# Kernel optimization log

Hardware: AMD Instinct MI355X
Metric: run time of the kernel (lower is better)

The kernel has to match this reference:

```python
import jax, jax.numpy as jnp
import numpy as np

B, T, H, W = 8, 16, 512, 512
N, C = 300000, 128
STRIDE_B, STRIDE_T, STRIDE_H = T * H * W, H * W, W
SENTINEL = B * STRIDE_B  # out-of-range linear index used as unique fill_value


def setup_inputs() -> dict:
    key = jax.random.key(0)
    ks = jax.random.split(key, 8)
    # Random valid voxel coordinates via decomposed random linear index
    lin = jax.random.randint(ks[0], (N,), 0, SENTINEL, dtype=jnp.int32)
    b = lin // STRIDE_B
    r = lin % STRIDE_B
    t = r // STRIDE_T
    r = r % STRIDE_T
    y = r // STRIDE_H
    x = r % STRIDE_H
    indices = jnp.stack([b, t, y, x], axis=1).astype(jnp.int32)  # [N,4]
    s = 0.02
    return {
        "feats": jax.random.normal(ks[1], (N, C), jnp.float32),
        "indices": indices,
        "W1": jax.random.normal(ks[2], (C, C), jnp.float32) * s,
        "ln1_g": jnp.ones((C,), jnp.float32),
        "ln1_b": jnp.zeros((C,), jnp.float32),
        "W2": jax.random.normal(ks[3], (C, C), jnp.float32) * s,
        "ln2_g": jnp.ones((C,), jnp.float32),
        "ln2_b": jnp.zeros((C,), jnp.float32),
        "se_w1": jax.random.normal(ks[4], (C, C // 4), jnp.float32) * s,
        "se_b1": jnp.zeros((C // 4,), jnp.float32),
        "se_w2": jax.random.normal(ks[5], (C // 4, C), jnp.float32) * s,
        "se_b2": jnp.zeros((C,), jnp.float32),
    }


def _layernorm(x, g, b, eps=1e-5):
    mu = jnp.mean(x, axis=-1, keepdims=True)
    var = jnp.mean((x - mu) ** 2, axis=-1, keepdims=True)
    return (x - mu) * jax.lax.rsqrt(var + eps) * g + b


def reference(feats, indices, W1, ln1_g, ln1_b, W2, ln2_g, ln2_b,
              se_w1, se_b1, se_w2, se_b2):
    # conv1 (SubMConv3d k=1 == per-voxel linear) -> LayerNorm -> ReLU
    out = jax.nn.relu(_layernorm(feats @ W1, ln1_g, ln1_b))
    # conv2 -> LayerNorm
    out = _layernorm(out @ W2, ln2_g, ln2_b)
    # SE: global mean over all voxels -> fc -> relu -> fc -> sigmoid -> scale
    squeezed = jnp.mean(out, axis=0)                       # [C]
    scale = jax.nn.sigmoid(jax.nn.relu(squeezed @ se_w1 + se_b1) @ se_w2 + se_b2)
    out = out * scale
    # sparse_add(out, identity): linear hash, unique, scatter_add
    idx = indices.astype(jnp.int32)
    lin = (idx[:, 0] * STRIDE_B + idx[:, 1] * STRIDE_T
           + idx[:, 2] * STRIDE_H + idx[:, 3])             # [N]
    all_lin = jnp.concatenate([lin, lin])                  # [2N]
    all_feats = jnp.concatenate([out, feats])              # [2N, C]
    M = all_lin.shape[0]
    uniq, inv = jnp.unique(all_lin, size=M, fill_value=SENTINEL,
                           return_inverse=True)
    inv = inv.ravel()
    merged = jax.ops.segment_sum(all_feats, inv, num_segments=M)  # [2N, C]
    # decompose unique linear indices back to (b, t, y, x)
    cb = uniq // STRIDE_B
    r = uniq % STRIDE_B
    ct = r // STRIDE_T
    r = r % STRIDE_T
    ch = r // STRIDE_H
    cw = r % STRIDE_H
    comb_idx = jnp.stack([cb, ct, ch, cw], axis=1).astype(jnp.int32)
    # drop zero-feature / padded voxels (fixed-shape mask instead of compaction)
    valid = (jnp.abs(merged).sum(axis=1) > 1e-8) & (uniq < SENTINEL)
    merged = jnp.where(valid[:, None], merged, 0.0)
    merged = jax.nn.relu(merged)                           # lif2
    return merged, comb_idx, valid
```

## Files before the change

kernel.cpp:

```cpp
#include <hip/hip_runtime.h>
#include <cstdint>
#include <cstddef>

#define NVOX 300000
#define SB 4194304
#define ST 262144
#define SHH 512
#define SENT 33554432
#define NWORDS (SENT/64)

typedef __attribute__((ext_vector_type(8))) short short8;
typedef __attribute__((ext_vector_type(4))) float f32x4;

static __device__ __forceinline__ float bf2f(unsigned short u){
  return __uint_as_float(((unsigned)u) << 16);
}
static __device__ __forceinline__ unsigned short f2bf(float f){
  unsigned u = __float_as_uint(f);
  u = u + 0x7fffu + ((u >> 16) & 1u);
  return (unsigned short)(u >> 16);
}
static __device__ __forceinline__ short8 pack8(float4 a, float4 b){
  short8 s;
  s[0]=(short)f2bf(a.x); s[1]=(short)f2bf(a.y); s[2]=(short)f2bf(a.z); s[3]=(short)f2bf(a.w);
  s[4]=(short)f2bf(b.x); s[5]=(short)f2bf(b.y); s[6]=(short)f2bf(b.z); s[7]=(short)f2bf(b.w);
  return s;
}

static __device__ __forceinline__ unsigned rank_of(int l,
    const unsigned long long* __restrict__ bits,
    const unsigned* __restrict__ coarse,
    const unsigned* __restrict__ blockExcl){
  int w = l >> 6;
  unsigned long long m = 1ull << (l & 63);
  return coarse[w] + blockExcl[w >> 12]
       + (unsigned)__popcll(bits[w] & (m - 1ull));
}

__global__ void pack_w(const float* __restrict__ W, unsigned short* __restrict__ Wt){
  int i = blockIdx.x*256 + threadIdx.x;
  int j = i & 7, lane = (i >> 3) & 63, ks = (i >> 9) & 3, nt = i >> 11;
  int k = ks*32 + (lane >> 4)*8 + j;
  int n = nt*16 + (lane & 15);
  Wt[i] = f2bf(W[k*128 + n]);
}

__global__ void mark_kernel(const int* __restrict__ idx,
                            unsigned long long* __restrict__ bits,
                            unsigned long long* __restrict__ dupbits,
                            int* __restrict__ lin,
                            int* __restrict__ duplist,
                            int* __restrict__ dupcount){
  int i = blockIdx.x*256 + threadIdx.x;
  if(i >= NVOX) return;
  int4 v = ((const int4*)idx)[i];
  int l = v.x*SB + v.y*ST + v.z*SHH + v.w;
  lin[i] = l;
  unsigned long long m = 1ull << (l & 63);
  unsigned long long old = atomicOr(&bits[l >> 6], m);
  if(old & m){
    atomicOr(&dupbits[l >> 6], m);
    int s = atomicAdd(dupcount, 1);
    duplist[s] = i;
  }
}

__global__ void scan1_kernel(const unsigned long long* __restrict__ bits,
                             unsigned* __restrict__ coarse,
                             unsigned* __restrict__ blockSums){
  __shared__ unsigned sh[256];
  int t = threadIdx.x, blk = blockIdx.x;
  int w0 = blk*4096 + t*16;
  unsigned p[16]; unsigned s = 0;
  #pragma unroll
  for(int k=0;k<16;k++){ unsigned c = (unsigned)__popcll(bits[w0+k]); p[k] = s; s += c; }
  sh[t] = s; __syncthreads();
  for(int off=1; off<256; off<<=1){
    unsigned v = (t >= off) ? sh[t-off] : 0u;
    __syncthreads();
    sh[t] += v;
    __syncthreads();
  }
  unsigned texcl = (t == 0) ? 0u : sh[t-1];
  #pragma unroll
  for(int k=0;k<16;k++) coarse[w0+k] = texcl + p[k];
  if(t == 255) blockSums[blk] = sh[255];
}

__global__ void scan2_kernel(const unsigned* __restrict__ blockSums,
                             unsigned* __restrict__ blockExcl){
  __shared__ unsigned sh[128];
  int t = threadIdx.x;
  sh[t] = blockSums[t]; __syncthreads();
  for(int off=1; off<128; off<<=1){
    unsigned v = (t >= off) ? sh[t-off] : 0u;
    __syncthreads();
    sh[t] += v;
    __syncthreads();
  }
  if(t == 0) blockExcl[0] = 0u;
  blockExcl[t+1] = sh[t];
}

__global__ void emit_kernel(const unsigned long long* __restrict__ bits,
                            const unsigned* __restrict__ coarse,
                            const unsigned* __restrict__ blockExcl,
                            float* __restrict__ out_comb){
  int w = blockIdx.x*256 + threadIdx.x;
  if(w >= NWORDS) return;
  unsigned long long bw = bits[w];
  if(!bw) return;
  unsigned j = coarse[w] + blockExcl[w >> 12];
  while(bw){
    int p = __builtin_ctzll(bw);
    bw &= bw - 1;
    int v = (w << 6) | p;
    int cb = v >> 22;
    int r  = v & (SB - 1);
    int ct = r >> 18;
    r &= (ST - 1);
    int ch = r >> 9;
    int cw = r & 511;
    ((float4*)out_comb)[j] = make_float4((float)cb,(float)ct,(float)ch,(float)cw);
    j++;
  }
}

__global__ void zerodup_kernel(const int* __restrict__ duplist,
    const int* __restrict__ dupcount, const int* __restrict__ lin,
    const unsigned long long* __restrict__ bits,
    const unsigned* __restrict__ coarse, const unsigned* __restrict__ blockExcl,
    float* __restrict__ out_merged)
{
  int cnt = *dupcount;
  int lane = threadIdx.x & 63;
  for(int e = blockIdx.x*4 + (threadIdx.x >> 6); e < cnt; e += gridDim.x*4){
    int l = lin[duplist[e]];
    unsigned j = rank_of(l, bits, coarse, blockExcl);
    *(float2*)(out_merged + (size_t)j*128 + 2*lane) = make_float2(0.f, 0.f);
  }
}

#define MLP_ROWS 128
__global__ __launch_bounds__(256) void fused_mlp(
    const float* __restrict__ X,
    const unsigned short* __restrict__ w1t, const float* __restrict__ g1v,
    const float* __restrict__ b1v,
    const unsigned short* __restrict__ w2t, const float* __restrict__ g2v,
    const float* __restrict__ b2v,
    unsigned short* __restrict__ Y, float* __restrict__ sq, int nrows)
{
  __shared__ __align__(16) unsigned short wlds[16384];
  __shared__ __align__(16) unsigned short xs[128][136];
  __shared__ float sqs[4][128];
  const int t = threadIdx.x;
  const int rowbase = blockIdx.x * MLP_ROWS;
  const int wave = t >> 6, quad = (t >> 4) & 3, l15 = t & 15;
  const int wbase = wave * 32;
  const int lane8 = (t & 63) * 8;
  const int kofs = quad * 8;
  const int grow0 = rowbase + wbase + l15;
  const int grow1 = grow0 + 16;
  const bool rv0 = grow0 < nrows, rv1 = grow1 < nrows;

  #pragma unroll
  for (int m = 0; m < 8; m++)
    ((float4*)wlds)[m*256 + t] = ((const float4*)w1t)[m*256 + t];

  short8 a0,a1,a2,a3,a4,a5,a6,a7;
  {
    float4 z = make_float4(0.f,0.f,0.f,0.f);
    float4 u0=z,u1=z,u2=z,u3=z,u4=z,u5=z,u6=z,u7=z;
    float4 w0=z,w1=z,w2=z,w3=z,w4=z,w5=z,w6=z,w7=z;
    if (rv0) {
      const float* xp = X + (size_t)grow0 * 128 + kofs;
      u0 = ((const float4*)(xp      ))[0];
      u1 = ((const float4*)(xp +   4))[0];
      u2 = ((const float4*)(xp +  32))[0];
      u3 = ((const float4*)(xp +  36))[0];
      u4 = ((const float4*)(xp +  64))[0];
      u5 = ((const float4*)(xp +  68))[0];
      u6 = ((const float4*)(xp +  96))[0];
      u7 = ((const float4*)(xp + 100))[0];
    }
    if (rv1) {
      const float* xp = X + (size_t)grow1 * 128 + kofs;
      w0 = ((const float4*)(xp      ))[0];
      w1 = ((const float4*)(xp +   4))[0];
      w2 = ((const float4*)(xp +  32))[0];
      w3 = ((const float4*)(xp +  36))[0];
      w4 = ((const float4*)(xp +  64))[0];
      w5 = ((const float4*)(xp +  68))[0];
      w6 = ((const float4*)(xp +  96))[0];
      w7 = ((const float4*)(xp + 100))[0];
    }
    a0 = pack8(u0, u1); a1 = pack8(u2, u3);
    a2 = pack8(u4, u5); a3 = pack8(u6, u7);
    a4 = pack8(w0, w1); a5 = pack8(w2, w3);
    a6 = pack8(w4, w5); a7 = pack8(w6, w7);
  }
  __syncthreads();

  {
    f32x4 acc0[8], acc1[8];
    #pragma unroll
    for (int nt = 0; nt < 8; nt++) {
      const unsigned short* wp = wlds + nt*2048 + lane8;
      short8 bv0 = *(const short8*)(wp);
      short8 bv1 = *(const short8*)(wp + 512);
      short8 bv2 = *(const short8*)(wp + 1024);
      short8 bv3 = *(const short8*)(wp + 1536);
      f32x4 c0 = {0.f,0.f,0.f,0.f}, c1 = {0.f,0.f,0.f,0.f};
      c0 = __builtin_amdgcn_mfma_f32_16x16x32_bf16(a0, bv0, c0, 0, 0, 0);
      c1 = __builtin_amdgcn_mfma_f32_16x16x32_bf16(a4, bv0, c1, 0, 0, 0);
      c0 = __builtin_amdgcn_mfma_f32_16x16x32_bf16(a1, bv1, c0, 0, 0, 0);
      c1 = __builtin_amdgcn_mfma_f32_16x16x32_bf16(a5, bv1, c1, 0, 0, 0);
      c0 = __builtin_amdgcn_mfma_f32_16x16x32_bf16(a2, bv2, c0, 0, 0, 0);
      c1 = __builtin_amdgcn_mfma_f32_16x16x32_bf16(a6, bv2, c1, 0, 0, 0);
      c0 = __builtin_amdgcn_mfma_f32_16x16x32_bf16(a3, bv3, c0, 0, 0, 0);
      c1 = __builtin_amdgcn_mfma_f32_16x16x32_bf16(a7, bv3, c1, 0, 0, 0);
      acc0[nt] = c0; acc1[nt] = c1;
    }

    float gg[8], bb[8];
    #pragma unroll
    for (int nt = 0; nt < 8; nt++) {
      gg[nt] = g1v[nt*16 + l15]; bb[nt] = b1v[nt*16 + l15];
    }
    #pragma unroll
    for (int tile = 0; tile < 2; tile++) {
      #pragma unroll
      for (int r = 0; r < 4; r++) {
        float s = 0.f, q = 0.f;
        #pragma unroll
        for (int nt = 0; nt < 8; nt++) {
          float v = tile ? acc1[nt][r] : acc0[nt][r]; s += v; q += v*v;
        }
        #pragma unroll
        for (int mm = 1; mm < 16; mm <<= 1) { s += __shfl_xor(s, mm); q += __shfl_xor(q, mm); }
        float mu = s * (1.f/128.f);
        float var = fmaxf(q * (1.f/128.f) - mu*mu, 0.f);
        float rinv = rsqrtf(var + 1e-5f);
        int orow = wbase + tile*16 + quad*4 + r;
        #pragma unroll
        for (int nt = 0; nt < 8; nt++) {
          float v = ((tile ? acc1[nt][r] : acc0[nt][r]) - mu) * rinv * gg[nt] + bb[nt];
          v = fmaxf(v, 0.f);
          xs[orow][nt*16 + l15] = f2bf(v);
        }
      }
    }
  }
  __syncthreads();

  #pragma unroll
  for (int m = 0; m < 8; m++)
    ((float4*)wlds)[m*256 + t] = ((const float4*)w2t)[m*256 + t];

  short8 p0 = *(const short8*)&xs[wbase + l15][  0 + kofs];
  short8 p1 = *(const short8*)&xs[wbase + l15][ 32 + kofs];
  short8 p2 = *(const short8*)&xs[wbase + l15][ 64 + kofs];
  short8 p3 = *(const short8*)&xs[wbase + l15][ 96 + kofs];
  short8 p4 = *(const short8*)&xs[wbase + 16 + l15][  0 + kofs];
  short8 p5 = *(const short8*)&xs[wbase + 16 + l15][ 32 + kofs];
  short8 p6 = *(const short8*)&xs[wbase + 16 + l15][ 64 + kofs];
  short8 p7 = *(const short8*)&xs[wbase + 16 + l15][ 96 + kofs];
  __syncthreads();

  {
    f32x4 acc0[8], acc1[8];
    #pragma unroll
    for (int nt = 0; nt < 8; nt++) {
      const unsigned short* wp = wlds + nt*2048 + lane8;
      short8 bv0 = *(const short8*)(wp);
      short8 bv1 = *(const short8*)(wp + 512);
      short8 bv2 = *(const short8*)(wp + 1024);
      short8 bv3 = *(const short8*)(wp + 1536);
      f32x4 c0 = {0.f,0.f,0.f,0.f}, c1 = {0.f,0.f,0.f,0.f};
      c0 = __builtin_amdgcn_mfma_f32_16x16x32_bf16(p0, bv0, c0, 0, 0, 0);
      c1 = __builtin_amdgcn_mfma_f32_16x16x32_bf16(p4, bv0, c1, 0, 0, 0);
      c0 = __builtin_amdgcn_mfma_f32_16x16x32_bf16(p1, bv1, c0, 0, 0, 0);
      c1 = __builtin_amdgcn_mfma_f32_16x16x32_bf16(p5, bv1, c1, 0, 0, 0);
      c0 = __builtin_amdgcn_mfma_f32_16x16x32_bf16(p2, bv2, c0, 0, 0, 0);
      c1 = __builtin_amdgcn_mfma_f32_16x16x32_bf16(p6, bv2, c1, 0, 0, 0);
      c0 = __builtin_amdgcn_mfma_f32_16x16x32_bf16(p3, bv3, c0, 0, 0, 0);
      c1 = __builtin_amdgcn_mfma_f32_16x16x32_bf16(p7, bv3, c1, 0, 0, 0);
      acc0[nt] = c0; acc1[nt] = c1;
    }

    float gg[8], bb[8], ch[8];
    #pragma unroll
    for (int nt = 0; nt < 8; nt++) {
      gg[nt] = g2v[nt*16 + l15]; bb[nt] = b2v[nt*16 + l15]; ch[nt] = 0.f;
    }
    #pragma unroll
    for (int tile = 0; tile < 2; tile++) {
      #pragma unroll
      for (int r = 0; r < 4; r++) {
        float s = 0.f, q = 0.f;
        #pragma unroll
        for (int nt = 0; nt < 8; nt++) {
          float v = tile ? acc1[nt][r] : acc0[nt][r]; s += v; q += v*v;
        }
        #pragma unroll
        for (int mm = 1; mm < 16; mm <<= 1) { s += __shfl_xor(s, mm); q += __shfl_xor(q, mm); }
        float mu = s * (1.f/128.f);
        float var = fmaxf(q * (1.f/128.f) - mu*mu, 0.f);
        float rinv = rsqrtf(var + 1e-5f);
        int orow = wbase + tile*16 + quad*4 + r;
        bool rv = (rowbase + orow) < nrows;
        #pragma unroll
        for (int nt = 0; nt < 8; nt++) {
          float v = ((tile ? acc1[nt][r] : acc0[nt][r]) - mu) * rinv * gg[nt] + bb[nt];
          if (rv) ch[nt] += v;
          xs[orow][nt*16 + l15] = f2bf(v);
        }
      }
    }
    #pragma unroll
    for (int nt = 0; nt < 8; nt++) {
      float v = ch[nt];
      v += __shfl_xor(v, 16); v += __shfl_xor(v, 32);
      if (quad == 0) sqs[wave][nt*16 + l15] = v;
    }
  }

  #pragma unroll
  for (int mm = 0; mm < 8; mm++) {
    int c = mm*64 + (t & 63);
    int rl = wbase + (c >> 4), s8 = c & 15;
    if (rowbase + rl < nrows) {
      short8 v = *(const short8*)&xs[rl][s8*8];
      *(short8*)(Y + (size_t)(rowbase+rl)*128 + s8*8) = v;
    }
  }
  __syncthreads();
  if (t < 128) atomicAdd(&sq[t], sqs[0][t] + sqs[1][t] + sqs[2][t] + sqs[3][t]);
}

__global__ void se_kernel(const float* __restrict__ sq, const float* __restrict__ w1,
    const float* __restrict__ b1, const float* __restrict__ w2,
    const float* __restrict__ b2, float* __restrict__ scale)
{
  __shared__ float mean[128];
  __shared__ float h1[32];
  int t = threadIdx.x;
  mean[t] = sq[t] * (1.f/(float)NVOX);
  __syncthreads();
  if(t < 32){
    float s = b1[t];
    for(int c=0;c<128;c++) s += mean[c]*w1[c*32+t];
    h1[t] = fmaxf(s, 0.f);
  }
  __syncthreads();
  float s = b2[t];
  for(int j=0;j<32;j++) s += h1[j]*w2[j*128+t];
  scale[t] = 1.f/(1.f + expf(-s));
}

__global__ void scatter_kernel(const unsigned short* __restrict__ y2,
    const float* __restrict__ feats, const float* __restrict__ scale,
    const int* __restrict__ lin, const unsigned long long* __restrict__ bits,
    const unsigned long long* __restrict__ dupbits,
    const unsigned* __restrict__ coarse, const unsigned* __restrict__ blockExcl,
    float* __restrict__ out_merged, float* __restrict__ out_valid)
{
  int row = blockIdx.x*4 + (threadIdx.x >> 6);
  int lane = threadIdx.x & 63;
  int l = lin[row];
  int w = l >> 6;
  unsigned long long m = 1ull << (l & 63);
  unsigned j = coarse[w] + blockExcl[w >> 12]
             + (unsigned)__popcll(bits[w] & (m - 1ull));
  size_t rb = (size_t)row * 128;
  unsigned yy = *(const unsigned*)(y2 + rb + 2*lane);
  float2 ff = *(const float2*)(feats + rb + 2*lane);
  float2 ss = *(const float2*)(scale + 2*lane);
  float v0 = bf2f((unsigned short)(yy & 0xffffu)) * ss.x + ff.x;
  float v1 = bf2f((unsigned short)(yy >> 16))     * ss.y + ff.y;
  size_t ob = (size_t)j * 128;
  if (dupbits[w] & m) {
    atomicAdd(out_merged + ob + 2*lane,     v0);
    atomicAdd(out_merged + ob + 2*lane + 1, v1);
  } else {
    float s = fabsf(v0) + fabsf(v1);
    #pragma unroll
    for(int mm=1; mm<64; mm<<=1) s += __shfl_xor(s, mm);
    bool valid = s > 1e-8f;
    float2 o;
    o.x = valid ? fmaxf(v0, 0.f) : 0.f;
    o.y = valid ? fmaxf(v1, 0.f) : 0.f;
    *(float2*)(out_merged + ob + 2*lane) = o;
    if (lane == 0) out_valid[j] = valid ? 1.f : 0.f;
  }
}

__global__ void dupfinal_kernel(const int* __restrict__ duplist,
    const int* __restrict__ dupcount, const int* __restrict__ lin,
    unsigned long long* __restrict__ dupbits,
    const unsigned long long* __restrict__ bits,
    const unsigned* __restrict__ coarse, const unsigned* __restrict__ blockExcl,
    float* __restrict__ out_merged, float* __restrict__ out_valid)
{
  int cnt = *dupcount;
  int lane = threadIdx.x & 63;
  for(int e = blockIdx.x*4 + (threadIdx.x >> 6); e < cnt; e += gridDim.x*4){
    int l = lin[duplist[e]];
    int w = l >> 6;
    unsigned long long m = 1ull << (l & 63);
    int claimed = 0;
    if (lane == 0){
      unsigned long long old = atomicAnd(&dupbits[w], ~m);
      claimed = (old & m) ? 1 : 0;
    }
    claimed = __shfl(claimed, 0);
    if (!claimed) continue;
    unsigned j = coarse[w] + blockExcl[w >> 12]
               + (unsigned)__popcll(bits[w] & (m - 1ull));
    size_t ob = (size_t)j * 128;
    float2 v = *(float2*)(out_merged + ob + 2*lane);
    float s = fabsf(v.x) + fabsf(v.y);
    #pragma unroll
    for(int mm=1; mm<64; mm<<=1) s += __shfl_xor(s, mm);
    bool valid = s > 1e-8f;
    float2 o;
    o.x = valid ? fmaxf(v.x, 0.f) : 0.f;
    o.y = valid ? fmaxf(v.y, 0.f) : 0.f;
    *(float2*)(out_merged + ob + 2*lane) = o;
    if (lane == 0) out_valid[j] = valid ? 1.f : 0.f;
  }
}

__global__ void padfill_kernel(const unsigned* __restrict__ blockExcl,
    float* __restrict__ out_merged, float* __restrict__ out_comb,
    float* __restrict__ out_valid)
{
  int lane = threadIdx.x & 63;
  int wv = threadIdx.x >> 6;
  if (blockIdx.x < 512) {
    unsigned U = blockExcl[128];
    for (unsigned r = U + blockIdx.x*4 + wv; r < NVOX; r += 512*4) {
      *(float2*)(out_merged + (size_t)r*128 + 2*lane) = make_float2(0.f, 0.f);
      if (lane == 0) {
        out_valid[r] = 0.f;
        ((float4*)out_comb)[r] = make_float4(8.f, 0.f, 0.f, 0.f);
      }
    }
  } else {
    int r = NVOX + (blockIdx.x - 512)*4 + wv;
    *(float2*)(out_merged + (size_t)r*128 + 2*lane) = make_float2(0.f, 0.f);
    if (lane == 0) {
      out_valid[r] = 0.f;
      ((float4*)out_comb)[r] = make_float4(8.f, 0.f, 0.f, 0.f);
    }
  }
}

extern "C" void kernel_launch(void* const* d_in, const int* in_sizes, int n_in,
                              void* d_out, int out_size, void* d_ws, size_t ws_size,
                              hipStream_t stream)
{
  const float* feats   = (const float*)d_in[0];
  const int*   indices = (const int*)d_in[1];
  const float* W1  = (const float*)d_in[2];
  const float* g1  = (const float*)d_in[3];
  const float* b1  = (const float*)d_in[4];
  const float* W2  = (const float*)d_in[5];
  const float* g2  = (const float*)d_in[6];
  const float* b2  = (const float*)d_in[7];
  const float* sw1 = (const float*)d_in[8];
  const float* sb1 = (const float*)d_in[9];
  const float* sw2 = (const float*)d_in[10];
  const float* sb2 = (const float*)d_in[11];

  float* out_merged = (float*)d_out;
  float* out_comb   = out_merged + (size_t)2*NVOX*128;
  float* out_valid  = out_comb   + (size_t)2*NVOX*4;

  char* cur = (char*)d_ws;
  auto alloc = [&](size_t b) -> void* {
    void* p = (void*)cur;
    cur += (b + 255) & ~(size_t)255;
    return p;
  };
  unsigned short*      y2        = (unsigned short*)alloc((size_t)NVOX*128*2);
  unsigned long long*  bits      = (unsigned long long*)alloc((size_t)NWORDS*8);
  unsigned long long*  dupbits   = (unsigned long long*)alloc((size_t)NWORDS*8);
  unsigned*            coarse    = (unsigned*)alloc((size_t)NWORDS*4);
  unsigned*            blockSums = (unsigned*)alloc(128*4);
  unsigned*            blockExcl = (unsigned*)alloc(129*4);
  float*               sq        = (float*)alloc(128*4);
  int*                 dupcount  = (int*)alloc(4);
  float*               scale     = (float*)alloc(128*4);
  int*                 lin       = (int*)alloc((size_t)NVOX*4);
  int*                 duplist   = (int*)alloc((size_t)NVOX*4);
  unsigned short*      w1t       = (unsigned short*)alloc(128*128*2);
  unsigned short*      w2t       = (unsigned short*)alloc(128*128*2);

  hipMemsetAsync(bits, 0, (size_t)NWORDS*8*2, stream);
  hipMemsetAsync(sq, 0, 512 + 256, stream);

  pack_w<<<64, 256, 0, stream>>>(W1, w1t);
  pack_w<<<64, 256, 0, stream>>>(W2, w2t);

  mark_kernel<<<(NVOX+255)/256, 256, 0, stream>>>(indices, bits, dupbits, lin,
                                                  duplist, dupcount);
  scan1_kernel<<<128, 256, 0, stream>>>(bits, coarse, blockSums);
  scan2_kernel<<<1, 128, 0, stream>>>(blockSums, blockExcl);
  emit_kernel<<<NWORDS/256, 256, 0, stream>>>(bits, coarse, blockExcl, out_comb);
  zerodup_kernel<<<512, 256, 0, stream>>>(duplist, dupcount, lin, bits, coarse,
                                          blockExcl, out_merged);

  fused_mlp<<<(NVOX + MLP_ROWS - 1)/MLP_ROWS, 256, 0, stream>>>(
      feats, w1t, g1, b1, w2t, g2, b2, y2, sq, NVOX);
  se_kernel<<<1, 128, 0, stream>>>(sq, sw1, sb1, sw2, sb2, scale);

  scatter_kernel<<<NVOX/4, 256, 0, stream>>>(y2, feats, scale, lin, bits, dupbits,
                                             coarse, blockExcl, out_merged, out_valid);
  dupfinal_kernel<<<512, 256, 0, stream>>>(duplist, dupcount, lin, dupbits, bits,
                                           coarse, blockExcl, out_merged, out_valid);
  padfill_kernel<<<512 + NVOX/4, 256, 0, stream>>>(blockExcl, out_merged,
                                                   out_comb, out_valid);
}
```

Measured before the change: 619.6 us.

## Merge small kernels, prefetch W2 into registers, spread SE atomics

Several independent changes. Adjacent small kernels are merged into single launches by block range: the two weight packs, emit with zerodup, and dupfinal with padfill. The SE column-sum atomics are spread over 32 buckets to cut contention, and se_kernel now sums the buckets. W2 is prefetched into registers at the start of fused_mlp so its load overlaps the first GEMM, and f32-to-bf16 conversion now uses the compiler's __bf16 cast. The costs are higher register pressure in fused_mlp and a slightly larger memset.

```diff
diff --git a/kernel.cpp b/kernel.cpp
--- a/kernel.cpp
+++ b/kernel.cpp
@@ -8,17 +8,18 @@
 #define SHH 512
 #define SENT 33554432
 #define NWORDS (SENT/64)
+#define SQB 32
 
 typedef __attribute__((ext_vector_type(8))) short short8;
 typedef __attribute__((ext_vector_type(4))) float f32x4;
 
+static __device__ __forceinline__ unsigned short f2bf(float f){
+  union { __bf16 b; unsigned short u; } c;
+  c.b = (__bf16)f;
+  return c.u;
+}
 static __device__ __forceinline__ float bf2f(unsigned short u){
   return __uint_as_float(((unsigned)u) << 16);
-}
-static __device__ __forceinline__ unsigned short f2bf(float f){
-  unsigned u = __float_as_uint(f);
-  u = u + 0x7fffu + ((u >> 16) & 1u);
-  return (unsigned short)(u >> 16);
 }
 static __device__ __forceinline__ short8 pack8(float4 a, float4 b){
   short8 s;
@@ -37,8 +38,12 @@
        + (unsigned)__popcll(bits[w] & (m - 1ull));
 }
 
-__global__ void pack_w(const float* __restrict__ W, unsigned short* __restrict__ Wt){
-  int i = blockIdx.x*256 + threadIdx.x;
+__global__ void pack_w2(const float* __restrict__ W1, const float* __restrict__ W2,
+                        unsigned short* __restrict__ W1t, unsigned short* __restrict__ W2t){
+  int gi = blockIdx.x*256 + threadIdx.x;
+  const float* W = (gi < 16384) ? W1 : W2;
+  unsigned short* Wt = (gi < 16384) ? W1t : W2t;
+  int i = gi & 16383;
   int j = i & 7, lane = (i >> 3) & 63, ks = (i >> 9) & 3, nt = i >> 11;
   int k = ks*32 + (lane >> 4)*8 + j;
   int n = nt*16 + (lane & 15);
@@ -102,42 +107,41 @@
   blockExcl[t+1] = sh[t];
 }
 
-__global__ void emit_kernel(const unsigned long long* __restrict__ bits,
+__global__ void emit_zerodup_kernel(const unsigned long long* __restrict__ bits,
                             const unsigned* __restrict__ coarse,
                             const unsigned* __restrict__ blockExcl,
-                            float* __restrict__ out_comb){
-  int w = blockIdx.x*256 + threadIdx.x;
-  if(w >= NWORDS) return;
-  unsigned long long bw = bits[w];
-  if(!bw) return;
-  unsigned j = coarse[w] + blockExcl[w >> 12];
-  while(bw){
-    int p = __builtin_ctzll(bw);
-    bw &= bw - 1;
-    int v = (w << 6) | p;
-    int cb = v >> 22;
-    int r  = v & (SB - 1);
-    int ct = r >> 18;
-    r &= (ST - 1);
-    int ch = r >> 9;
-    int cw = r & 511;
-    ((float4*)out_comb)[j] = make_float4((float)cb,(float)ct,(float)ch,(float)cw);
-    j++;
-  }
-}
-
-__global__ void zerodup_kernel(const int* __restrict__ duplist,
-    const int* __restrict__ dupcount, const int* __restrict__ lin,
-    const unsigned long long* __restrict__ bits,
-    const unsigned* __restrict__ coarse, const unsigned* __restrict__ blockExcl,
-    float* __restrict__ out_merged)
-{
-  int cnt = *dupcount;
-  int lane = threadIdx.x & 63;
-  for(int e = blockIdx.x*4 + (threadIdx.x >> 6); e < cnt; e += gridDim.x*4){
-    int l = lin[duplist[e]];
-    unsigned j = rank_of(l, bits, coarse, blockExcl);
-    *(float2*)(out_merged + (size_t)j*128 + 2*lane) = make_float2(0.f, 0.f);
+                            float* __restrict__ out_comb,
+                            const int* __restrict__ duplist,
+                            const int* __restrict__ dupcount,
+                            const int* __restrict__ lin,
+                            float* __restrict__ out_merged){
+  if (blockIdx.x < 2048) {
+    int w = blockIdx.x*256 + threadIdx.x;
+    unsigned long long bw = bits[w];
+    if(!bw) return;
+    unsigned j = coarse[w] + blockExcl[w >> 12];
+    while(bw){
+      int p = __builtin_ctzll(bw);
+      bw &= bw - 1;
+      int v = (w << 6) | p;
+      int cb = v >> 22;
+      int r  = v & (SB - 1);
+      int ct = r >> 18;
+      r &= (ST - 1);
+      int ch = r >> 9;
+      int cw = r & 511;
+      ((float4*)out_comb)[j] = make_float4((float)cb,(float)ct,(float)ch,(float)cw);
+      j++;
+    }
+  } else {
+    int cnt = *dupcount;
+    int lane = threadIdx.x & 63;
+    int base = (blockIdx.x - 2048)*4 + (threadIdx.x >> 6);
+    for(int e = base; e < cnt; e += 512*4){
+      int l = lin[duplist[e]];
+      unsigned j = rank_of(l, bits, coarse, blockExcl);
+      *(float2*)(out_merged + (size_t)j*128 + 2*lane) = make_float2(0.f, 0.f);
+    }
   }
 }
 
@@ -148,7 +152,7 @@
     const float* __restrict__ b1v,
     const unsigned short* __restrict__ w2t, const float* __restrict__ g2v,
     const float* __restrict__ b2v,
-    unsigned short* __restrict__ Y, float* __restrict__ sq, int nrows)
+    unsigned short* __restrict__ Y, float* __restrict__ sqb, int nrows)
 {
   __shared__ __align__(16) unsigned short wlds[16384];
   __shared__ __align__(16) unsigned short xs[128][136];
@@ -166,6 +170,11 @@
   #pragma unroll
   for (int m = 0; m < 8; m++)
     ((float4*)wlds)[m*256 + t] = ((const float4*)w1t)[m*256 + t];
+
+  float4 wreg[8];
+  #pragma unroll
+  for (int m = 0; m < 8; m++)
+    wreg[m] = ((const float4*)w2t)[m*256 + t];
 
   short8 a0,a1,a2,a3,a4,a5,a6,a7;
   {
@@ -255,7 +264,7 @@
 
   #pragma unroll
   for (int m = 0; m < 8; m++)
-    ((float4*)wlds)[m*256 + t] = ((const float4*)w2t)[m*256 + t];
+    ((float4*)wlds)[m*256 + t] = wreg[m];
 
   short8 p0 = *(const short8*)&xs[wbase + l15][  0 + kofs];
   short8 p1 = *(const short8*)&xs[wbase + l15][ 32 + kofs];
@@ -335,17 +344,22 @@
     }
   }
   __syncthreads();
-  if (t < 128) atomicAdd(&sq[t], sqs[0][t] + sqs[1][t] + sqs[2][t] + sqs[3][t]);
-}
-
-__global__ void se_kernel(const float* __restrict__ sq, const float* __restrict__ w1,
+  if (t < 128)
+    atomicAdd(&sqb[(blockIdx.x & (SQB-1))*128 + t],
+              sqs[0][t] + sqs[1][t] + sqs[2][t] + sqs[3][t]);
+}
+
+__global__ void se_kernel(const float* __restrict__ sqb, const float* __restrict__ w1,
     const float* __restrict__ b1, const float* __restrict__ w2,
     const float* __restrict__ b2, float* __restrict__ scale)
 {
   __shared__ float mean[128];
   __shared__ float h1[32];
   int t = threadIdx.x;
-  mean[t] = sq[t] * (1.f/(float)NVOX);
+  float acc = 0.f;
+  #pragma unroll
+  for (int k = 0; k < SQB; k++) acc += sqb[k*128 + t];
+  mean[t] = acc * (1.f/(float)NVOX);
   __syncthreads();
   if(t < 32){
     float s = b1[t];
@@ -395,51 +409,47 @@
   }
 }
 
-__global__ void dupfinal_kernel(const int* __restrict__ duplist,
+__global__ void dupfinal_pad_kernel(const int* __restrict__ duplist,
     const int* __restrict__ dupcount, const int* __restrict__ lin,
     unsigned long long* __restrict__ dupbits,
     const unsigned long long* __restrict__ bits,
     const unsigned* __restrict__ coarse, const unsigned* __restrict__ blockExcl,
-    float* __restrict__ out_merged, float* __restrict__ out_valid)
-{
-  int cnt = *dupcount;
-  int lane = threadIdx.x & 63;
-  for(int e = blockIdx.x*4 + (threadIdx.x >> 6); e < cnt; e += gridDim.x*4){
-    int l = lin[duplist[e]];
-    int w = l >> 6;
-    unsigned long long m = 1ull << (l & 63);
-    int claimed = 0;
-    if (lane == 0){
-      unsigned long long old = atomicAnd(&dupbits[w], ~m);
-      claimed = (old & m) ? 1 : 0;
-    }
-    claimed = __shfl(claimed, 0);
-    if (!claimed) continue;
-    unsigned j = coarse[w] + blockExcl[w >> 12]
-               + (unsigned)__popcll(bits[w] & (m - 1ull));
-    size_t ob = (size_t)j * 128;
-    float2 v = *(float2*)(out_merged + ob + 2*lane);
-    float s = fabsf(v.x) + fabsf(v.y);
-    #pragma unroll
-    for(int mm=1; mm<64; mm<<=1) s += __shfl_xor(s, mm);
-    bool valid = s > 1e-8f;
-    float2 o;
-    o.x = valid ? fmaxf(v.x, 0.f) : 0.f;
-    o.y = valid ? fmaxf(v.y, 0.f) : 0.f;
-    *(float2*)(out_merged + ob + 2*lane) = o;
-    if (lane == 0) out_valid[j] = valid ? 1.f : 0.f;
-  }
-}
-
-__global__ void padfill_kernel(const unsigned* __restrict__ blockExcl,
-    float* __restrict__ out_merged, float* __restrict__ out_comb,
-    float* __restrict__ out_valid)
+    float* __restrict__ out_merged, float* __restrict__ out_valid,
+    float* __restrict__ out_comb)
 {
   int lane = threadIdx.x & 63;
   int wv = threadIdx.x >> 6;
-  if (blockIdx.x < 512) {
+  unsigned b = blockIdx.x;
+  if (b < 512) {
+    int cnt = *dupcount;
+    for(int e = b*4 + wv; e < cnt; e += 512*4){
+      int l = lin[duplist[e]];
+      int w = l >> 6;
+      unsigned long long m = 1ull << (l & 63);
+      int claimed = 0;
+      if (lane == 0){
+        unsigned long long old = atomicAnd(&dupbits[w], ~m);
+        claimed = (old & m) ? 1 : 0;
+      }
+      claimed = __shfl(claimed, 0);
+      if (!claimed) continue;
+      unsigned j = coarse[w] + blockExcl[w >> 12]
+                 + (unsigned)__popcll(bits[w] & (m - 1ull));
+      size_t ob = (size_t)j * 128;
+      float2 v = *(float2*)(out_merged + ob + 2*lane);
+      float s = fabsf(v.x) + fabsf(v.y);
+      #pragma unroll
+      for(int mm=1; mm<64; mm<<=1) s += __shfl_xor(s, mm);
+      bool valid = s > 1e-8f;
+      float2 o;
+      o.x = valid ? fmaxf(v.x, 0.f) : 0.f;
+      o.y = valid ? fmaxf(v.y, 0.f) : 0.f;
+      *(float2*)(out_merged + ob + 2*lane) = o;
+      if (lane == 0) out_valid[j] = valid ? 1.f : 0.f;
+    }
+  } else if (b < 1024) {
     unsigned U = blockExcl[128];
-    for (unsigned r = U + blockIdx.x*4 + wv; r < NVOX; r += 512*4) {
+    for (unsigned r = U + (b - 512)*4 + wv; r < NVOX; r += 512*4) {
       *(float2*)(out_merged + (size_t)r*128 + 2*lane) = make_float2(0.f, 0.f);
       if (lane == 0) {
         out_valid[r] = 0.f;
@@ -447,7 +457,7 @@
       }
     }
   } else {
-    int r = NVOX + (blockIdx.x - 512)*4 + wv;
+    int r = NVOX + (b - 1024)*4 + wv;
     *(float2*)(out_merged + (size_t)r*128 + 2*lane) = make_float2(0.f, 0.f);
     if (lane == 0) {
       out_valid[r] = 0.f;
@@ -489,7 +499,7 @@
   unsigned*            coarse    = (unsigned*)alloc((size_t)NWORDS*4);
   unsigned*            blockSums = (unsigned*)alloc(128*4);
   unsigned*            blockExcl = (unsigned*)alloc(129*4);
-  float*               sq        = (float*)alloc(128*4);
+  float*               sqb       = (float*)alloc(SQB*128*4);
   int*                 dupcount  = (int*)alloc(4);
   float*               scale     = (float*)alloc(128*4);
   int*                 lin       = (int*)alloc((size_t)NVOX*4);
@@ -498,27 +508,23 @@
   unsigned short*      w2t       = (unsigned short*)alloc(128*128*2);
 
   hipMemsetAsync(bits, 0, (size_t)NWORDS*8*2, stream);
-  hipMemsetAsync(sq, 0, 512 + 256, stream);
-
-  pack_w<<<64, 256, 0, stream>>>(W1, w1t);
-  pack_w<<<64, 256, 0, stream>>>(W2, w2t);
+  hipMemsetAsync(sqb, 0, SQB*128*4 + 256, stream);
+
+  pack_w2<<<128, 256, 0, stream>>>(W1, W2, w1t, w2t);
 
   mark_kernel<<<(NVOX+255)/256, 256, 0, stream>>>(indices, bits, dupbits, lin,
                                                   duplist, dupcount);
   scan1_kernel<<<128, 256, 0, stream>>>(bits, coarse, blockSums);
   scan2_kernel<<<1, 128, 0, stream>>>(blockSums, blockExcl);
-  emit_kernel<<<NWORDS/256, 256, 0, stream>>>(bits, coarse, blockExcl, out_comb);
-  zerodup_kernel<<<512, 256, 0, stream>>>(duplist, dupcount, lin, bits, coarse,
-                                          blockExcl, out_merged);
+  emit_zerodup_kernel<<<2560, 256, 0, stream>>>(bits, coarse, blockExcl, out_comb,
+                                                duplist, dupcount, lin, out_merged);
 
   fused_mlp<<<(NVOX + MLP_ROWS - 1)/MLP_ROWS, 256, 0, stream>>>(
-      feats, w1t, g1, b1, w2t, g2, b2, y2, sq, NVOX);
-  se_kernel<<<1, 128, 0, stream>>>(sq, sw1, sb1, sw2, sb2, scale);
+      feats, w1t, g1, b1, w2t, g2, b2, y2, sqb, NVOX);
+  se_kernel<<<1, 128, 0, stream>>>(sqb, sw1, sb1, sw2, sb2, scale);
 
   scatter_kernel<<<NVOX/4, 256, 0, stream>>>(y2, feats, scale, lin, bits, dupbits,
                                              coarse, blockExcl, out_merged, out_valid);
-  dupfinal_kernel<<<512, 256, 0, stream>>>(duplist, dupcount, lin, dupbits, bits,
-                                           coarse, blockExcl, out_merged, out_valid);
-  padfill_kernel<<<512 + NVOX/4, 256, 0, stream>>>(blockExcl, out_merged,
-                                                   out_comb, out_valid);
-}
+  dupfinal_pad_kernel<<<1024 + NVOX/4, 256, 0, stream>>>(duplist, dupcount, lin,
+      dupbits, bits, coarse, blockExcl, out_merged, out_valid, out_comb);
+}
```

After: 612.9 us. About the same (-1.1%).
